# Performance work log

Hardware: AMD Instinct MI355X
Metric: run time of the kernel (lower is better)

Reference implementation:

```python
import jax, jax.numpy as jnp
from jax import lax
import numpy as np

LAG, IN, H, B, T = 168, 64, 1024, 512, 168

def setup_inputs() -> dict:
    key = jax.random.key(0)
    ks = jax.random.split(key, 10)
    s1 = 1.0 / np.sqrt(LAG)
    sg = 1.0 / np.sqrt(H)
    return {
        "lag": jax.random.normal(ks[0], (B, LAG), jnp.float32),
        "curr": jax.random.normal(ks[1], (T, B, IN), jnp.float32),
        "W1": jax.random.uniform(ks[2], (H, LAG), jnp.float32, -s1, s1),
        "b1": jax.random.uniform(ks[3], (H,), jnp.float32, -s1, s1),
        "W_ih": jax.random.uniform(ks[4], (3 * H, IN), jnp.float32, -sg, sg),
        "b_ih": jax.random.uniform(ks[5], (3 * H,), jnp.float32, -sg, sg),
        "W_hh": jax.random.uniform(ks[6], (3 * H, H), jnp.float32, -sg, sg),
        "b_hh": jax.random.uniform(ks[7], (3 * H,), jnp.float32, -sg, sg),
        "W3": jax.random.uniform(ks[8], (1, H), jnp.float32, -sg, sg),
        "b3": jax.random.uniform(ks[9], (1,), jnp.float32, -sg, sg),
    }

def reference(lag, curr, W1, b1, W_ih, b_ih, W_hh, b_hh, W3, b3):
    # h_t = dense1(lag)
    h0 = lag @ W1.T + b1  # [B, H]

    def step(h, x):
        # PyTorch GRUCell math
        gi = x @ W_ih.T + b_ih   # [B, 3H]
        gh = h @ W_hh.T + b_hh   # [B, 3H]
        i_r, i_z, i_n = jnp.split(gi, 3, axis=-1)
        h_r, h_z, h_n = jnp.split(gh, 3, axis=-1)
        r = jax.nn.sigmoid(i_r + h_r)
        z = jax.nn.sigmoid(i_z + h_z)
        n = jnp.tanh(i_n + r * h_n)
        h_new = (1.0 - z) * n + z * h
        y = h_new @ W3.T + b3    # [B, 1] -> dense3 prediction
        return h_new, y[:, 0]

    _, ys = lax.scan(step, h0, curr)  # ys: [T, B]
    # torch.stack(outputs, 1).squeeze(2) -> [B, T]
    return ys.T
```

## Files before the change

kernel.cpp:

```cpp
#include <hip/hip_runtime.h>

#define T_STEPS 168
#define B_SZ 512
#define H_SZ 1024
#define IN_SZ 64
#define LAG_SZ 168
#define NWG 256
#define TPB 256

typedef __attribute__((ext_vector_type(8))) short short8;
typedef __attribute__((ext_vector_type(8))) __bf16 bf16x8;
typedef __attribute__((ext_vector_type(4))) float floatx4;

union V8u { short8 s; bf16x8 v; unsigned u[4]; };

__device__ __forceinline__ float bf2f(unsigned short u) {
    union { unsigned u; float f; } v; v.u = ((unsigned)u) << 16; return v.f;
}
__device__ __forceinline__ unsigned short f2bf(float x) {
    union { float f; unsigned u; } v; v.f = x;
    unsigned r = ((v.u >> 16) & 1u) + 0x7fffu;
    return (unsigned short)((v.u + r) >> 16);
}
__device__ __forceinline__ unsigned cvtpk(float a, float b) {
    unsigned r; asm("v_cvt_pk_bf16_f32 %0, %1, %2" : "=v"(r) : "v"(a), "v"(b)); return r;
}
__device__ __forceinline__ float lo_f(unsigned u) {
    union { unsigned x; float f; } v; v.x = u << 16; return v.f;
}
__device__ __forceinline__ float hi_f(unsigned u) {
    union { unsigned x; float f; } v; v.x = u & 0xffff0000u; return v.f;
}

#define MFB(a, b, c) __builtin_amdgcn_mfma_f32_16x16x32_bf16((a), (b), (c), 0, 0, 0)


__global__ void crnn_init2(const float* __restrict__ Whh,
                           unsigned short* __restrict__ whi,
                           unsigned short* __restrict__ h_hi,
                           unsigned short* __restrict__ ypart,
                           unsigned int* __restrict__ flg, unsigned int* __restrict__ pop)
{
    int tid = blockIdx.x * blockDim.x + threadIdx.x;
    int nthr = gridDim.x * blockDim.x;
    for (int c = tid; c < 64 * 96 * 64; c += nthr) {
        int lane = c & 63;
        int f = (c >> 6) % 96;
        int n16 = c / (96 * 64);
        int kk = f / 3, g = f % 3;
        int l15 = lane & 15, g4 = lane >> 4;
        int row = g * H_SZ + n16 * 16 + l15;
        int col = kk * 32 + g4 * 8;
        const float* src = Whh + (size_t)row * H_SZ + col;
        short8 sh;
        #pragma unroll
        for (int e = 0; e < 8; e++) sh[e] = (short)f2bf(src[e]);
        *(short8*)(whi + (size_t)c * 8) = sh;
    }
    for (int k = tid; k < 2 * B_SZ * H_SZ; k += nthr) h_hi[k] = 0;
    for (int k = tid; k < 168 * 8 * 64 * 32; k += nthr) ypart[k] = 0;
    for (int k = tid; k < 169 * 1024; k += nthr) flg[k] = 0u;
    for (int k = tid; k < 16; k += nthr) pop[k] = 0u;
}

#define ISSUE_A(ARR, KB) { \
    unsigned va_ = voffA_cur + (unsigned)((KB) * 512); \
    asm volatile("global_load_dwordx4 %0, %1, %2 sc0"            : "=v"(ARR[0].s) : "v"(va_), "s"(sAh)); \
    asm volatile("global_load_dwordx4 %0, %1, %2 offset:64 sc0"  : "=v"(ARR[1].s) : "v"(va_), "s"(sAh)); \
    asm volatile("global_load_dwordx4 %0, %1, %2 offset:128 sc0" : "=v"(ARR[2].s) : "v"(va_), "s"(sAh)); \
    asm volatile("global_load_dwordx4 %0, %1, %2 offset:192 sc0" : "=v"(ARR[3].s) : "v"(va_), "s"(sAh)); \
    asm volatile("global_load_dwordx4 %0, %1, %2 offset:256 sc0" : "=v"(ARR[4].s) : "v"(va_), "s"(sAh)); \
    asm volatile("global_load_dwordx4 %0, %1, %2 offset:320 sc0" : "=v"(ARR[5].s) : "v"(va_), "s"(sAh)); \
    asm volatile("global_load_dwordx4 %0, %1, %2 offset:384 sc0" : "=v"(ARR[6].s) : "v"(va_), "s"(sAh)); \
    asm volatile("global_load_dwordx4 %0, %1, %2 offset:448 sc0" : "=v"(ARR[7].s) : "v"(va_), "s"(sAh)); \
}

#define KEEP8(ARR) { \
    _Pragma("unroll") \
    for (int _q = 0; _q < 8; _q++) asm volatile("" : "+v"(ARR[_q].s)); \
}

#define COMPUTE_G(ARR, KB) { \
    _Pragma("unroll") \
    for (int q = 0; q < 8; q++) { \
        const int kk = (KB) * 8 + q; \
        unsigned o_ = (unsigned)(kk * 64); \
        bf16x8 xA0 = *(const bf16x8*)((const char*)whhA + ((bb0 + o_) ^ swz)); \
        bf16x8 xA1 = *(const bf16x8*)((const char*)whhA + ((bb1 + o_) ^ swz)); \
        bf16x8 xA2 = *(const bf16x8*)((const char*)whhA + ((bb2 + o_) ^ swz)); \
        const char* pB = wfB + (size_t)kk * 3072; \
        bf16x8 h1_0 = *(const bf16x8*)(pB); \
        bf16x8 h1_1 = *(const bf16x8*)(pB + 1024); \
        bf16x8 h1_2 = *(const bf16x8*)(pB + 2048); \
        acc[0] = MFB(ARR[q].v, xA0, acc[0]); \
        acc[2] = MFB(ARR[q].v, xA1, acc[2]); \
        acc[4] = MFB(ARR[q].v, xA2, acc[4]); \
        acc[1] = MFB(ARR[q].v, h1_0, acc[1]); \
        acc[3] = MFB(ARR[q].v, h1_1, acc[3]); \
        acc[5] = MFB(ARR[q].v, h1_2, acc[5]); \
    } \
}

__launch_bounds__(TPB, 1)
__global__ void crnn_main2(
    const float* __restrict__ lag, const float* __restrict__ curr,
    const float* __restrict__ W1, const float* __restrict__ b1,
    const float* __restrict__ Wih, const float* __restrict__ b_ih,
    const float* __restrict__ Whh, const float* __restrict__ b_hh,
    const float* __restrict__ W3, const float* __restrict__ b3,
    const unsigned short* __restrict__ whi,
    unsigned short* __restrict__ h_hi, unsigned short* __restrict__ ypart,
    unsigned int* __restrict__ flg, unsigned int* __restrict__ pop,
    float* __restrict__ out)
{
    __shared__ __align__(16) unsigned short whhA[48 * 1024];
    __shared__ __align__(16) unsigned short wihh[96 * 64];
    __shared__ __align__(16) unsigned short wihl[96 * 64];
    __shared__ int sh_xr[2];

    const int tid = threadIdx.x;
    if (tid == 0) {
        unsigned x;
        asm volatile("s_getreg_b32 %0, hwreg(HW_REG_XCC_ID)" : "=s"(x));
        x &= 7u;
        unsigned rk = __hip_atomic_fetch_add(&pop[x], 1u, __ATOMIC_RELAXED, __HIP_MEMORY_SCOPE_AGENT);
        sh_xr[0] = (int)x;
        sh_xr[1] = (int)(rk & 31u);
    }
    __syncthreads();
    const int xcc = sh_xr[0];
    const int r = sh_xr[1];
    const int RB = xcc * 64;
    const int J = r * 32;
    const int n16B = 2 * r + 1;

    const int lane = tid & 63;
    const int wv = tid >> 6;
    const int l15 = lane & 15;
    const int g4 = lane >> 4;

    for (int c = tid; c < 48 * 128; c += TPB) {
        int rr = c >> 7, cc = c & 127;
        int gr = (rr >> 4) * H_SZ + J + (rr & 15);
        const float* src = Whh + (size_t)gr * H_SZ + cc * 8;
        short8 s;
        #pragma unroll
        for (int e = 0; e < 8; e++) s[e] = (short)f2bf(src[e]);
        unsigned byte = ((unsigned)(rr * 2048 + cc * 16)) ^ ((unsigned)((rr & 7) << 4));
        *(short8*)((char*)whhA + byte) = s;
    }
    for (int c = tid; c < 96 * 8; c += TPB) {
        int rr = c >> 3, cc = c & 7;
        int gr = (rr >> 5) * H_SZ + J + (rr & 31);
        const float* src = Wih + (size_t)gr * IN_SZ + cc * 8;
        short8 sh, sl;
        #pragma unroll
        for (int e = 0; e < 8; e++) {
            float v = src[e];
            unsigned short hi = f2bf(v);
            sh[e] = (short)hi;
            sl[e] = (short)f2bf(v - bf2f(hi));
        }
        unsigned byte = ((unsigned)(rr * 128 + cc * 16)) ^ ((unsigned)((rr & 7) << 4));
        *(short8*)((char*)wihh + byte) = sh;
        *(short8*)((char*)wihl + byte) = sl;
    }
    __syncthreads();

    bool dead = false;
    auto set_flag_wave = [&](int t1) {
        asm volatile("s_waitcnt vmcnt(0)" ::: "memory");
        if (lane == 0)
            __hip_atomic_store(flg + (size_t)t1 * 1024 + (size_t)xcc * 128 + (size_t)r * 4 + wv,
                               1u, __ATOMIC_RELAXED, __HIP_MEMORY_SCOPE_AGENT);
    };
    auto check = [&](int t, int kb) {
        if (dead) { __builtin_amdgcn_sched_barrier(0); return; }
        const unsigned int* fp = flg + (size_t)t * 1024 + (size_t)xcc * 128
                               + (size_t)(kb * 8 + (lane & 7)) * 4 + wv;
        int spins = 0;
        while (true) {
            unsigned v = __hip_atomic_load(fp, __ATOMIC_RELAXED, __HIP_MEMORY_SCOPE_AGENT);
            if (__ballot(v != 0) == ~0ull) break;
            __builtin_amdgcn_s_sleep(1);
            if (++spins > 2000000) { dead = true; break; }
        }
        __builtin_amdgcn_sched_barrier(0);
    };

    float hp[2][4];
    {
        const int brow = RB + wv * 16 + g4 * 4;
        #pragma unroll
        for (int j16 = 0; j16 < 2; j16++) {
            const int j = J + j16 * 16 + l15;
            float a[4];
            float bias = b1[j];
            #pragma unroll
            for (int e = 0; e < 4; e++) a[e] = bias;
            const float* w1p = W1 + (size_t)j * LAG_SZ;
            for (int k = 0; k < LAG_SZ; k += 4) {
                floatx4 w4 = *(const floatx4*)(w1p + k);
                #pragma unroll
                for (int e = 0; e < 4; e++) {
                    floatx4 l4 = *(const floatx4*)(lag + (size_t)(brow + e) * LAG_SZ + k);
                    a[e] += l4.x * w4.x + l4.y * w4.y + l4.z * w4.z + l4.w * w4.w;
                }
            }
            #pragma unroll
            for (int e = 0; e < 4; e++) {
                hp[j16][e] = a[e];
                h_hi[(size_t)(brow + e) * H_SZ + j] = f2bf(a[e]);
            }
        }
    }
    set_flag_wave(0);

    float br_[2], bz_[2], bni_[2], bnh_[2];
    #pragma unroll
    for (int j16 = 0; j16 < 2; j16++) {
        int j = J + j16 * 16 + l15;
        br_[j16] = b_ih[j] + b_hh[j];
        bz_[j16] = b_ih[H_SZ + j] + b_hh[H_SZ + j];
        bni_[j16] = b_ih[2 * H_SZ + j];
        bnh_[j16] = b_hh[2 * H_SZ + j];
    }
    const float w3a = W3[J + l15];
    const float w3b = W3[J + 16 + l15];
    const float b3v = b3[0];

    const unsigned short* sAh = h_hi;
    const char* wfB = (const char*)whi + (size_t)n16B * 98304 + lane * 16;
    const unsigned voffA0 = (unsigned)(((RB + wv * 16 + l15) * H_SZ + g4 * 8) * 2);

    const unsigned bb0 = (unsigned)((0 * 16 + l15) * 2048 + g4 * 16);
    const unsigned bb1 = (unsigned)((1 * 16 + l15) * 2048 + g4 * 16);
    const unsigned bb2 = (unsigned)((2 * 16 + l15) * 2048 + g4 * 16);
    const unsigned swz = (unsigned)((l15 & 7) << 4);

    floatx4 acc_gi[6];
    auto compute_gi = [&](int t) {
        const float* xp = curr + (size_t)t * (B_SZ * IN_SZ)
                        + (size_t)(RB + wv * 16 + l15) * IN_SZ + g4 * 8;
        #pragma unroll
        for (int ni = 0; ni < 6; ni++) acc_gi[ni] = floatx4{0.f, 0.f, 0.f, 0.f};
        #pragma unroll
        for (int kg = 0; kg < 2; kg++) {
            floatx4 v0 = *(const floatx4*)(xp + kg * 32);
            floatx4 v1 = *(const floatx4*)(xp + kg * 32 + 4);
            V8u ah, al;
            ah.u[0] = cvtpk(v0.x, v0.y); ah.u[1] = cvtpk(v0.z, v0.w);
            ah.u[2] = cvtpk(v1.x, v1.y); ah.u[3] = cvtpk(v1.z, v1.w);
            al.u[0] = cvtpk(v0.x - lo_f(ah.u[0]), v0.y - hi_f(ah.u[0]));
            al.u[1] = cvtpk(v0.z - lo_f(ah.u[1]), v0.w - hi_f(ah.u[1]));
            al.u[2] = cvtpk(v1.x - lo_f(ah.u[2]), v1.y - hi_f(ah.u[2]));
            al.u[3] = cvtpk(v1.z - lo_f(ah.u[3]), v1.w - hi_f(ah.u[3]));
            #pragma unroll
            for (int g = 0; g < 3; g++) {
                #pragma unroll
                for (int j16 = 0; j16 < 2; j16++) {
                    int rr = g * 32 + j16 * 16 + l15;
                    unsigned byte = ((unsigned)(rr * 128 + kg * 64 + g4 * 16)) ^ ((unsigned)((rr & 7) << 4));
                    bf16x8 bh = *(const bf16x8*)((const char*)wihh + byte);
                    bf16x8 bl = *(const bf16x8*)((const char*)wihl + byte);
                    int ni = g * 2 + j16;
                    acc_gi[ni] = MFB(ah.v, bh, acc_gi[ni]);
                    acc_gi[ni] = MFB(al.v, bh, acc_gi[ni]);
                    acc_gi[ni] = MFB(ah.v, bl, acc_gi[ni]);
                }
            }
        }
    };

    compute_gi(0);

    const int kb0 = r >> 3;
    int cur = 0;
    for (int t = 0; t < T_STEPS; t++) {
        const unsigned voffA_cur = voffA0 + (unsigned)cur * 1048576u;

        floatx4 acc[6];
        #pragma unroll
        for (int ni = 0; ni < 6; ni++) acc[ni] = floatx4{0.f, 0.f, 0.f, 0.f};

        V8u A0[8], A1[8];
        const int k0 = kb0, k1 = (kb0 + 1) & 3, k2 = (kb0 + 2) & 3, k3 = (kb0 + 3) & 3;

        check(t, k0); ISSUE_A(A0, k0);
        check(t, k1); ISSUE_A(A1, k1);
        KEEP8(A0);  COMPUTE_G(A0, k0);
        check(t, k2); ISSUE_A(A0, k2);
        KEEP8(A1);  COMPUTE_G(A1, k1);
        check(t, k3); ISSUE_A(A1, k3);
        KEEP8(A0);  COMPUTE_G(A0, k2);
        asm volatile("s_waitcnt vmcnt(0)" ::: "memory");
        __builtin_amdgcn_sched_barrier(0);
        KEEP8(A1);  COMPUTE_G(A1, k3);

        {
            unsigned short* nh = h_hi + (size_t)(cur ^ 1) * 524288;
            const int brow = RB + wv * 16 + g4 * 4;
            #pragma unroll
            for (int j16 = 0; j16 < 2; j16++) {
                const int j = J + j16 * 16 + l15;
                #pragma unroll
                for (int e = 0; e < 4; e++) {
                    float grv = acc[0 + j16][e] + acc_gi[0 + j16][e] + br_[j16];
                    float gzv = acc[2 + j16][e] + acc_gi[2 + j16][e] + bz_[j16];
                    float ghn = acc[4 + j16][e] + bnh_[j16];
                    float gin = acc_gi[4 + j16][e] + bni_[j16];
                    float rg = 1.f / (1.f + __expf(-grv));
                    float zg = 1.f / (1.f + __expf(-gzv));
                    float nx = gin + rg * ghn;
                    float e2 = __expf(-2.f * fabsf(nx));
                    float th = copysignf((1.f - e2) / (1.f + e2), nx);
                    float hnew = (1.f - zg) * th + zg * hp[j16][e];
                    hp[j16][e] = hnew;
                    nh[(size_t)(brow + e) * H_SZ + j] = f2bf(hnew);
                }
            }
        }

        if (t + 1 < T_STEPS) set_flag_wave(t + 1);

        {
            #pragma unroll
            for (int e = 0; e < 4; e++) {
                float p = w3a * hp[0][e] + w3b * hp[1][e];
                p += __shfl_xor(p, 1, 64);
                p += __shfl_xor(p, 2, 64);
                p += __shfl_xor(p, 4, 64);
                p += __shfl_xor(p, 8, 64);
                if (l15 == 0) {
                    int row = wv * 16 + g4 * 4 + e;
                    ypart[((size_t)(t * 8 + xcc) * 64 + row) * 32 + r] = f2bf(p);
                }
            }
        }

        if (t + 1 < T_STEPS) compute_gi(t + 1);
        cur ^= 1;
    }

    set_flag_wave(T_STEPS);
    {
        if (!dead) {
            const unsigned int* f1 = flg + (size_t)T_STEPS * 1024 + (size_t)xcc * 128 + lane;
            const unsigned int* f2 = f1 + 64;
            int spins = 0;
            while (true) {
                unsigned v1 = __hip_atomic_load(f1, __ATOMIC_RELAXED, __HIP_MEMORY_SCOPE_AGENT);
                unsigned v2 = __hip_atomic_load(f2, __ATOMIC_RELAXED, __HIP_MEMORY_SCOPE_AGENT);
                if (__ballot(v1 != 0) == ~0ull && __ballot(v2 != 0) == ~0ull) break;
                __builtin_amdgcn_s_sleep(1);
                if (++spins > 2000000) { dead = true; break; }
            }
        }
        __builtin_amdgcn_sched_barrier(0);
    }

    for (int q = tid; q < 2 * T_STEPS; q += TPB) {
        int t = q >> 1;
        int rowq = 2 * r + (q & 1);
        const char* yp = (const char*)(ypart + ((size_t)(t * 8 + xcc) * 64 + rowq) * 32);
        V8u v0, v1, v2, v3;
        asm volatile("global_load_dwordx4 %0, %1, off sc0" : "=v"(v0.s) : "v"(yp));
        asm volatile("global_load_dwordx4 %0, %1, off offset:16 sc0" : "=v"(v1.s) : "v"(yp));
        asm volatile("global_load_dwordx4 %0, %1, off offset:32 sc0" : "=v"(v2.s) : "v"(yp));
        asm volatile("global_load_dwordx4 %0, %1, off offset:48 sc0" : "=v"(v3.s) : "v"(yp));
        asm volatile("s_waitcnt vmcnt(0)" ::: "memory");
        __builtin_amdgcn_sched_barrier(0);
        float s = b3v;
        #pragma unroll
        for (int e = 0; e < 8; e++) {
            s += bf2f((unsigned short)v0.s[e]) + bf2f((unsigned short)v1.s[e])
               + bf2f((unsigned short)v2.s[e]) + bf2f((unsigned short)v3.s[e]);
        }
        out[(size_t)(RB + rowq) * T_STEPS + t] = s;
    }
}


extern "C" void kernel_launch(void* const* d_in, const int* in_sizes, int n_in,
                              void* d_out, int out_size, void* d_ws, size_t ws_size,
                              hipStream_t stream) {
    const float* lag  = (const float*)d_in[0];
    const float* curr = (const float*)d_in[1];
    const float* W1   = (const float*)d_in[2];
    const float* b1   = (const float*)d_in[3];
    const float* Wih  = (const float*)d_in[4];
    const float* bih  = (const float*)d_in[5];
    const float* Whh  = (const float*)d_in[6];
    const float* bhh  = (const float*)d_in[7];
    const float* W3   = (const float*)d_in[8];
    const float* b3   = (const float*)d_in[9];
    float* out = (float*)d_out;
    char* w = (char*)d_ws;

    if (ws_size < (size_t)14585920) return;

    unsigned short* whi   = (unsigned short*)(w + 0);
    unsigned short* h_hi  = (unsigned short*)(w + 6291456);
    unsigned short* ypart = (unsigned short*)(w + 8388608);
    unsigned int*   flg   = (unsigned int*)(w + 13893632);
    unsigned int*   pop   = (unsigned int*)(w + 14585856);

    hipLaunchKernelGGL(crnn_init2, dim3(2048), dim3(256), 0, stream,
                       Whh, whi, h_hi, ypart, flg, pop);

    void* args[] = { (void*)&lag, (void*)&curr, (void*)&W1, (void*)&b1,
                     (void*)&Wih, (void*)&bih, (void*)&Whh, (void*)&bhh,
                     (void*)&W3, (void*)&b3, (void*)&whi,
                     (void*)&h_hi, (void*)&ypart, (void*)&flg, (void*)&pop, (void*)&out };
    hipError_t e = hipLaunchCooperativeKernel((void*)crnn_main2, dim3(NWG), dim3(TPB), args, 0, stream);
    if (e != hipSuccess) {
        (void)hipGetLastError();
        hipLaunchKernelGGL(crnn_main2, dim3(NWG), dim3(TPB), 0, stream,
                           lag, curr, W1, b1, Wih, bih, Whh, bhh, W3, b3,
                           whi, h_hi, ypart, flg, pop, out);
    }
}
```

Measured before the change: 2.686 ms.

## Use per-workgroup step flags and prefetch next step's first h tile

Cross-workgroup step flags move from per-wave granularity to one flag per workgroup, set after a __syncthreads, which reduces the number of flags each consumer polls. The spin loop no longer sleeps between polls. The first A-tile load for step t+1 is issued at the end of step t, and the loaded registers are hoisted out of the loop so that load latency overlaps the tail of the current step. The trade-off is an extra block-wide barrier per step, more aggressive polling traffic, and coarser dependency tracking.

```diff
diff --git a/kernel.cpp b/kernel.cpp
--- a/kernel.cpp
+++ b/kernel.cpp
@@ -59,12 +59,12 @@
     }
     for (int k = tid; k < 2 * B_SZ * H_SZ; k += nthr) h_hi[k] = 0;
     for (int k = tid; k < 168 * 8 * 64 * 32; k += nthr) ypart[k] = 0;
-    for (int k = tid; k < 169 * 1024; k += nthr) flg[k] = 0u;
+    for (int k = tid; k < 169 * 256; k += nthr) flg[k] = 0u;
     for (int k = tid; k < 16; k += nthr) pop[k] = 0u;
 }
 
-#define ISSUE_A(ARR, KB) { \
-    unsigned va_ = voffA_cur + (unsigned)((KB) * 512); \
+#define ISSUE_A(ARR, KB, VB) { \
+    unsigned va_ = (VB) + (unsigned)((KB) * 512); \
     asm volatile("global_load_dwordx4 %0, %1, %2 sc0"            : "=v"(ARR[0].s) : "v"(va_), "s"(sAh)); \
     asm volatile("global_load_dwordx4 %0, %1, %2 offset:64 sc0"  : "=v"(ARR[1].s) : "v"(va_), "s"(sAh)); \
     asm volatile("global_load_dwordx4 %0, %1, %2 offset:128 sc0" : "=v"(ARR[2].s) : "v"(va_), "s"(sAh)); \
@@ -165,28 +165,6 @@
         *(short8*)((char*)wihh + byte) = sh;
         *(short8*)((char*)wihl + byte) = sl;
     }
-    __syncthreads();
-
-    bool dead = false;
-    auto set_flag_wave = [&](int t1) {
-        asm volatile("s_waitcnt vmcnt(0)" ::: "memory");
-        if (lane == 0)
-            __hip_atomic_store(flg + (size_t)t1 * 1024 + (size_t)xcc * 128 + (size_t)r * 4 + wv,
-                               1u, __ATOMIC_RELAXED, __HIP_MEMORY_SCOPE_AGENT);
-    };
-    auto check = [&](int t, int kb) {
-        if (dead) { __builtin_amdgcn_sched_barrier(0); return; }
-        const unsigned int* fp = flg + (size_t)t * 1024 + (size_t)xcc * 128
-                               + (size_t)(kb * 8 + (lane & 7)) * 4 + wv;
-        int spins = 0;
-        while (true) {
-            unsigned v = __hip_atomic_load(fp, __ATOMIC_RELAXED, __HIP_MEMORY_SCOPE_AGENT);
-            if (__ballot(v != 0) == ~0ull) break;
-            __builtin_amdgcn_s_sleep(1);
-            if (++spins > 2000000) { dead = true; break; }
-        }
-        __builtin_amdgcn_sched_barrier(0);
-    };
 
     float hp[2][4];
     {
@@ -214,7 +192,6 @@
             }
         }
     }
-    set_flag_wave(0);
 
     float br_[2], bz_[2], bni_[2], bnh_[2];
     #pragma unroll
@@ -237,6 +214,27 @@
     const unsigned bb1 = (unsigned)((1 * 16 + l15) * 2048 + g4 * 16);
     const unsigned bb2 = (unsigned)((2 * 16 + l15) * 2048 + g4 * 16);
     const unsigned swz = (unsigned)((l15 & 7) << 4);
+
+    bool dead = false;
+    auto set_flag = [&](int t1) {
+        asm volatile("s_waitcnt vmcnt(0)" ::: "memory");
+        __syncthreads();
+        if (tid == 0)
+            __hip_atomic_store(flg + (size_t)t1 * 256 + (size_t)xcc * 32 + (size_t)r, 1u,
+                               __ATOMIC_RELAXED, __HIP_MEMORY_SCOPE_AGENT);
+    };
+    auto check = [&](int t, int kb) {
+        if (dead) { __builtin_amdgcn_sched_barrier(0); return; }
+        const unsigned int* fp = flg + (size_t)t * 256 + (size_t)xcc * 32
+                               + (size_t)kb * 8 + (size_t)(lane & 7);
+        int spins = 0;
+        while (true) {
+            unsigned v = __hip_atomic_load(fp, __ATOMIC_RELAXED, __HIP_MEMORY_SCOPE_AGENT);
+            if (__ballot(v != 0) == ~0ull) break;
+            if (++spins > 2000000) { dead = true; break; }
+        }
+        __builtin_amdgcn_sched_barrier(0);
+    };
 
     floatx4 acc_gi[6];
     auto compute_gi = [&](int t) {
@@ -272,10 +270,16 @@
         }
     };
 
+    set_flag(0);
     compute_gi(0);
 
     const int kb0 = r >> 3;
+    const int k0 = kb0, k1 = (kb0 + 1) & 3, k2 = (kb0 + 2) & 3, k3 = (kb0 + 3) & 3;
+
+    V8u A0[8], A1[8];
     int cur = 0;
+    check(0, k0); ISSUE_A(A0, k0, voffA0);
+
     for (int t = 0; t < T_STEPS; t++) {
         const unsigned voffA_cur = voffA0 + (unsigned)cur * 1048576u;
 
@@ -283,15 +287,11 @@
         #pragma unroll
         for (int ni = 0; ni < 6; ni++) acc[ni] = floatx4{0.f, 0.f, 0.f, 0.f};
 
-        V8u A0[8], A1[8];
-        const int k0 = kb0, k1 = (kb0 + 1) & 3, k2 = (kb0 + 2) & 3, k3 = (kb0 + 3) & 3;
-
-        check(t, k0); ISSUE_A(A0, k0);
-        check(t, k1); ISSUE_A(A1, k1);
+        check(t, k1); ISSUE_A(A1, k1, voffA_cur);
         KEEP8(A0);  COMPUTE_G(A0, k0);
-        check(t, k2); ISSUE_A(A0, k2);
+        check(t, k2); ISSUE_A(A0, k2, voffA_cur);
         KEEP8(A1);  COMPUTE_G(A1, k1);
-        check(t, k3); ISSUE_A(A1, k3);
+        check(t, k3); ISSUE_A(A1, k3, voffA_cur);
         KEEP8(A0);  COMPUTE_G(A0, k2);
         asm volatile("s_waitcnt vmcnt(0)" ::: "memory");
         __builtin_amdgcn_sched_barrier(0);
@@ -321,8 +321,6 @@
             }
         }
 
-        if (t + 1 < T_STEPS) set_flag_wave(t + 1);
-
         {
             #pragma unroll
             for (int e = 0; e < 4; e++) {
@@ -338,27 +336,19 @@
             }
         }
 
-        if (t + 1 < T_STEPS) compute_gi(t + 1);
-        cur ^= 1;
-    }
-
-    set_flag_wave(T_STEPS);
-    {
-        if (!dead) {
-            const unsigned int* f1 = flg + (size_t)T_STEPS * 1024 + (size_t)xcc * 128 + lane;
-            const unsigned int* f2 = f1 + 64;
-            int spins = 0;
-            while (true) {
-                unsigned v1 = __hip_atomic_load(f1, __ATOMIC_RELAXED, __HIP_MEMORY_SCOPE_AGENT);
-                unsigned v2 = __hip_atomic_load(f2, __ATOMIC_RELAXED, __HIP_MEMORY_SCOPE_AGENT);
-                if (__ballot(v1 != 0) == ~0ull && __ballot(v2 != 0) == ~0ull) break;
-                __builtin_amdgcn_s_sleep(1);
-                if (++spins > 2000000) { dead = true; break; }
-            }
-        }
-        __builtin_amdgcn_sched_barrier(0);
-    }
-
+        set_flag(t + 1);
+
+        if (t + 1 < T_STEPS) {
+            compute_gi(t + 1);
+            cur ^= 1;
+            const unsigned voffA_nxt = voffA0 + (unsigned)cur * 1048576u;
+            check(t + 1, k0); ISSUE_A(A0, k0, voffA_nxt);
+        } else {
+            cur ^= 1;
+        }
+    }
+
+    check(T_STEPS, 0); check(T_STEPS, 1); check(T_STEPS, 2); check(T_STEPS, 3);
     for (int q = tid; q < 2 * T_STEPS; q += TPB) {
         int t = q >> 1;
         int rowq = 2 * r + (q & 1);
@@ -397,13 +387,13 @@
     float* out = (float*)d_out;
     char* w = (char*)d_ws;
 
-    if (ws_size < (size_t)14585920) return;
+    if (ws_size < (size_t)14066752) return;
 
     unsigned short* whi   = (unsigned short*)(w + 0);
     unsigned short* h_hi  = (unsigned short*)(w + 6291456);
     unsigned short* ypart = (unsigned short*)(w + 8388608);
     unsigned int*   flg   = (unsigned int*)(w + 13893632);
-    unsigned int*   pop   = (unsigned int*)(w + 14585856);
+    unsigned int*   pop   = (unsigned int*)(w + 14066688);
 
     hipLaunchKernelGGL(crnn_init2, dim3(2048), dim3(256), 0, stream,
                        Whh, whi, h_hi, ypart, flg, pop);
```

New measurement: 2.433 ms. 1.1x faster.
